# Optimization experiments

Hardware: AMD Instinct MI355X
Metric: run time of the kernel (lower is better)

## Reference

```python
import jax, jax.numpy as jnp
import numpy as np

B, N, COUT, CIN, H, W = 16, 4, 256, 256, 64, 64


def setup_inputs() -> dict:
    key = jax.random.key(0)
    k1, k2, k3, k4 = jax.random.split(key, 4)
    x = jax.random.normal(k1, (B, CIN, H, W), jnp.float32)
    alphas = jax.random.uniform(k2, (B, N), jnp.float32)          # routing weights (lambdas)
    angles = jax.random.normal(k3, (B, N), jnp.float32) * 0.5     # thetas, mixed signs
    # kaiming_normal_(mode='fan_out', relu): std = sqrt(2 / (Cout * k * k))
    std = np.sqrt(2.0 / (COUT * 9)).astype(np.float32)
    weight = jax.random.normal(k4, (N, COUT, CIN, 3, 3), jnp.float32) * std
    return {"x": x, "alphas": alphas, "angles": angles, "weight": weight}


def _rot_mats(thetas):
    """thetas: [M] -> rotation matrices [M, 9, 9] (row, col), matching torch builder."""
    xc = jnp.cos(thetas)
    ys = jnp.sin(thetas)
    a = xc - ys
    b = xc * ys
    c = xc + ys
    z = jnp.zeros_like(xc)
    o = jnp.ones_like(xc)

    def mat(rows):
        # rows: list of 9 lists of 9 [M]-arrays -> [M, 9, 9]
        return jnp.stack([jnp.stack(r, axis=-1) for r in rows], axis=-2)

    pos = mat([
        [a, 1 - a, z, z, z, z, z, z, z],
        [z, xc - b, b, z, 1 - c + b, ys - b, z, z, z],
        [z, z, a, z, z, 1 - a, z, z, z],
        [b, ys - b, z, xc - b, 1 - c + b, z, z, z, z],
        [z, z, z, z, o, z, z, z, z],
        [z, z, z, z, 1 - c + b, xc - b, z, ys - b, b],
        [z, z, z, 1 - a, z, z, a, z, z],
        [z, z, z, ys - b, 1 - c + b, z, b, xc - b, z],
        [z, z, z, z, z, z, z, 1 - a, a],
    ])
    neg = mat([
        [c, z, z, 1 - c, z, z, z, z, z],
        [-b, xc + b, z, b - ys, 1 - a - b, z, z, z, z],
        [z, 1 - c, c, z, z, z, z, z, z],
        [z, z, z, xc + b, 1 - a - b, z, -b, b - ys, z],
        [z, z, z, z, o, z, z, z, z],
        [z, b - ys, -b, z, 1 - a - b, xc + b, z, z, z],
        [z, z, z, z, z, z, c, 1 - c, z],
        [z, z, z, z, 1 - a - b, b - ys, z, xc + b, -b],
        [z, z, z, z, z, 1 - c, z, z, c],
    ])
    m = (thetas >= 0).astype(thetas.dtype)[:, None, None]
    return m * pos + (1 - m) * neg


def reference(x, alphas, angles, weight):
    bsz, Cin, h, w = x.shape
    n, Cout = weight.shape[0], weight.shape[1]
    # [bsz, n, 9, 9] rotation matrices scaled by routing lambdas
    rm = _rot_mats(angles.reshape(-1)).reshape(bsz, n, 9, 9)
    rm = rm * alphas[:, :, None, None]
    # weights [n, Cout, Cin, 3, 3] -> [n, 9, Cout*Cin]
    Wf = weight.transpose(0, 3, 4, 1, 2).reshape(n, 9, Cout * Cin)
    # mix over kernel_number n and source tap q -> per-sample rotated kernels
    rw = jnp.einsum('bnpq,nqm->bpm', rm, Wf)          # [bsz, 9, Cout*Cin]
    rw = rw.reshape(bsz, 3, 3, Cout, Cin).transpose(0, 3, 4, 1, 2)
    rw = rw.reshape(bsz * Cout, Cin, 3, 3)
    # per-sample conv via grouped conv on flattened batch
    xr = x.reshape(1, bsz * Cin, h, w)
    out = jax.lax.conv_general_dilated(
        xr, rw, window_strides=(1, 1), padding=((1, 1), (1, 1)),
        dimension_numbers=('NCHW', 'OIHW', 'NCHW'), feature_group_count=bsz)
    return out.reshape(bsz, Cout, out.shape[2], out.shape[3])
```

## Files before the change

kernel.cpp:

```cpp
#include <hip/hip_runtime.h>
#include <hip/hip_bf16.h>

#define B_    16
#define N_    4
#define COUT  256
#define CIN   256
#define H_    64
#define W_    64
#define K_TOT (CIN * 9)
#define HW    (H_ * W_)
#define NKT   72
#define PAD   66
#define PLANE (PAD * PAD)

typedef __attribute__((ext_vector_type(8))) short short8;
typedef __attribute__((ext_vector_type(4))) float f32x4;
typedef unsigned short ushort_t;

static __device__ __forceinline__ ushort_t f2bf(float f) {
    __hip_bfloat16 h = __float2bfloat16(f);
    return *reinterpret_cast<ushort_t*>(&h);
}

typedef __attribute__((address_space(3))) unsigned int lds_u32;
typedef __attribute__((address_space(1))) const unsigned int glb_u32;
static __device__ __forceinline__ void gl_lds16(const ushort_t* g, ushort_t* l) {
    __builtin_amdgcn_global_load_lds((glb_u32*)g, (lds_u32*)l, 16, 0, 0);
}

#define BARRIER() asm volatile("s_barrier" ::: "memory")
#define VMCNTN(N) asm volatile("s_waitcnt vmcnt(" #N ")" ::: "memory")

__global__ void rot_mats_kernel(const float* __restrict__ alphas,
                                const float* __restrict__ angles,
                                float* __restrict__ rm) {
    int i = threadIdx.x;
    if (i >= B_ * N_) return;
    float th = angles[i], al = alphas[i];
    float xc = cosf(th), ys = sinf(th);
    float a = xc - ys, b = xc * ys, c = xc + ys;
    float r[81];
#pragma unroll
    for (int j = 0; j < 81; ++j) r[j] = 0.f;
    if (th >= 0.f) {
        r[0] = a;          r[1] = 1.f - a;
        r[10] = xc - b;    r[11] = b;        r[13] = 1.f - c + b; r[14] = ys - b;
        r[20] = a;         r[23] = 1.f - a;
        r[27] = b;         r[28] = ys - b;   r[30] = xc - b;      r[31] = 1.f - c + b;
        r[40] = 1.f;
        r[49] = 1.f - c + b; r[50] = xc - b; r[52] = ys - b;      r[53] = b;
        r[57] = 1.f - a;   r[60] = a;
        r[66] = ys - b;    r[67] = 1.f - c + b; r[69] = b;        r[70] = xc - b;
        r[79] = 1.f - a;   r[80] = a;
    } else {
        r[0] = c;          r[3] = 1.f - c;
        r[9] = -b;         r[10] = xc + b;   r[12] = b - ys;      r[13] = 1.f - a - b;
        r[19] = 1.f - c;   r[20] = c;
        r[30] = xc + b;    r[31] = 1.f - a - b; r[33] = -b;       r[34] = b - ys;
        r[40] = 1.f;
        r[46] = b - ys;    r[47] = -b;       r[49] = 1.f - a - b; r[50] = xc + b;
        r[60] = c;         r[61] = 1.f - c;
        r[67] = 1.f - a - b; r[68] = b - ys; r[70] = xc + b;      r[71] = -b;
        r[77] = 1.f - c;   r[80] = c;
    }
#pragma unroll
    for (int j = 0; j < 81; ++j) rm[i * 81 + j] = r[j] * al;
}

__global__ __launch_bounds__(256)
void build_rw_kernel(const float* __restrict__ weight,
                     const float* __restrict__ rm,
                     ushort_t* __restrict__ rw) {
    __shared__ float rms[N_ * 81];
    int tid = threadIdx.x;
    int b = blockIdx.y;
    for (int j = tid; j < N_ * 81; j += 256)
        rms[j] = rm[b * N_ * 81 + j];
    __syncthreads();

    int idx = blockIdx.x * 256 + tid;
    int cout = idx >> 8, cin = idx & 255;

    float wv[N_][9];
#pragma unroll
    for (int n = 0; n < N_; ++n)
#pragma unroll
        for (int q = 0; q < 9; ++q)
            wv[n][q] = weight[(size_t)(n * (COUT * CIN) + idx) * 9 + q];

    ushort_t* dst = rw + (size_t)(b * COUT + cout) * K_TOT + cin;
#pragma unroll
    for (int p = 0; p < 9; ++p) {
        float s = 0.f;
#pragma unroll
        for (int n = 0; n < N_; ++n)
#pragma unroll
            for (int q = 0; q < 9; ++q)
                s += rms[n * 81 + p * 9 + q] * wv[n][q];
        dst[p * 256] = f2bf(s);
    }
}

__global__ __launch_bounds__(256)
void halo_zero_kernel(ushort_t* __restrict__ xt) {
    ushort_t* base = xt + (size_t)blockIdx.x * PLANE * 64;
    int t = threadIdx.x;
    for (int i = t; i < 260; i += 256) {
        int py, px;
        if (i < 66)       { py = 0;  px = i; }
        else if (i < 132) { py = 65; px = i - 66; }
        else if (i < 196) { py = i - 132 + 1; px = 0; }
        else              { py = i - 196 + 1; px = 65; }
        ushort_t* d = base + (size_t)(py * PAD + px) * 64;
        int4 z = {0, 0, 0, 0};
#pragma unroll
        for (int q = 0; q < 8; ++q) *(int4*)(d + q * 8) = z;
    }
}

__global__ __launch_bounds__(256)
void nhwc_kernel(const float* __restrict__ x, ushort_t* __restrict__ xt) {
    int y    = blockIdx.x;
    int cb32 = blockIdx.y;
    int b    = blockIdx.z;
    __shared__ ushort_t tileT[64][40];
    int t = threadIdx.x;

    int ci = t & 31, seg = t >> 5;
    const float* src = x + ((size_t)(b * CIN + cb32 * 32 + ci) * HW + y * 64 + seg * 8);
    float4 f0 = ((const float4*)src)[0];
    float4 f1 = ((const float4*)src)[1];
#pragma unroll
    for (int q = 0; q < 4; ++q) tileT[seg * 8 + q][ci]     = f2bf(((float*)&f0)[q]);
#pragma unroll
    for (int q = 0; q < 4; ++q) tileT[seg * 8 + 4 + q][ci] = f2bf(((float*)&f1)[q]);
    __syncthreads();

    int px = t >> 2, cseg = t & 3;
    ushort_t* dst = xt + ((size_t)(b * 4 + (cb32 >> 1)) * PLANE + (y + 1) * PAD + px + 1) * 64
                       + (cb32 & 1) * 32 + cseg * 8;
    *(int4*)dst = *(const int4*)&tileT[px][cseg * 8];
}

__global__ __launch_bounds__(512, 2)
void conv_kernel(const ushort_t* __restrict__ xt,
                 const ushort_t* __restrict__ rw,
                 float* __restrict__ out) {
    int bid0 = blockIdx.x;
    int bid = (bid0 & 7) * 32 + (bid0 >> 3);
    int b     = bid >> 4;
    int ptile = bid & 15;
    int y0 = ptile * 4;
    int tid = threadIdx.x;
    int lane = tid & 63, wid = tid >> 6;
    int wm = wid >> 2, wn = wid & 3;
    int rA = lane & 15, kseg = lane >> 4;

    __shared__ __align__(16) ushort_t As[3][8192];
    __shared__ __align__(16) ushort_t Bs[3][8192];
    ushort_t* AsB = &As[0][0];
    ushort_t* BsB = &Bs[0][0];

    f32x4 acc[8][4] = {};

    const ushort_t* rwb = rw + (size_t)b * COUT * K_TOT;
    const ushort_t* xtb = xt + ((size_t)b * 4 * PLANE + (size_t)y0 * PAD) * 64;

    int asrc[2], bsrc[2], uDst[2];
#pragma unroll
    for (int i = 0; i < 2; ++i) {
        int u = i * 512 + tid;
        int l = u >> 3, s = u & 7;
        int c = s ^ (l & 7);
        int row = 2 * l + (c >> 2);
        asrc[i] = row * K_TOT + (c & 3) * 8;
        bsrc[i] = ((row >> 6) * PAD + (row & 63)) * 64 + (c & 3) * 8;
        uDst[i] = u * 8;
    }
    const int slotR = (kseg + 4 * (rA & 1)) ^ ((rA >> 1) & 7);
    const int aRd = (wm * 64 + (rA >> 1)) * 64 + slotR * 8;
    const int bRd = (wn * 32 + (rA >> 1)) * 64 + slotR * 8;

#define STAGE_A(KT, Q)                                                         \
    {                                                                          \
        int p_ = (KT) >> 3, sub_ = (KT) & 7;                                   \
        int ako = p_ * 256 + sub_ * 32;                                        \
        gl_lds16(rwb + asrc[0] + ako, AsB + (Q) * 8192 + uDst[0]);             \
        gl_lds16(rwb + asrc[1] + ako, AsB + (Q) * 8192 + uDst[1]);             \
    }

#define STAGE_B(KT, Q)                                                         \
    {                                                                          \
        int p_ = (KT) >> 3, sub_ = (KT) & 7;                                   \
        int ph_ = p_ / 3, pw_ = p_ - 3 * ph_;                                  \
        const ushort_t* sb_ = xtb + (size_t)((sub_ >> 1) * PLANE + ph_ * PAD + pw_) * 64 \
                              + (sub_ & 1) * 32;                               \
        gl_lds16(sb_ + bsrc[0], BsB + (Q) * 8192 + uDst[0]);                   \
        gl_lds16(sb_ + bsrc[1], BsB + (Q) * 8192 + uDst[1]);                   \
    }

#define DO_MFMA(MH)                                                            \
    __builtin_amdgcn_s_setprio(1);                                             \
    _Pragma("unroll")                                                          \
    for (int mi = 0; mi < 4; ++mi)                                             \
        _Pragma("unroll")                                                      \
        for (int ni = 0; ni < 4; ++ni)                                         \
            acc[(MH) * 4 + mi][ni] = __builtin_amdgcn_mfma_f32_16x16x32_bf16(  \
                af[mi], bf[ni], acc[(MH) * 4 + mi][ni], 0, 0, 0);              \
    __builtin_amdgcn_s_setprio(0);

    STAGE_A(0, 0); STAGE_B(0, 0);
    STAGE_A(1, 1); STAGE_B(1, 1);
    VMCNTN(4);
    BARRIER();

    short8 af[4], bf[4];
    int qc = 0;
    for (int kt = 0; kt < NKT; ++kt) {
        int qs = qc + 2; if (qs >= 3) qs -= 3;
        bool more = (kt + 2 < NKT);
#pragma unroll
        for (int mi = 0; mi < 4; ++mi)
            af[mi] = *(const short8*)(AsB + qc * 8192 + aRd + mi * 512);
#pragma unroll
        for (int ni = 0; ni < 4; ++ni)
            bf[ni] = *(const short8*)(BsB + qc * 8192 + bRd + ni * 512);
        if (more) STAGE_A(kt + 2, qs);
        BARRIER();
        DO_MFMA(0);
        BARRIER();
#pragma unroll
        for (int mi = 0; mi < 4; ++mi)
            af[mi] = *(const short8*)(AsB + qc * 8192 + aRd + (mi + 4) * 512);
        if (more) STAGE_B(kt + 2, qs);
        BARRIER();
        DO_MFMA(1);
        if (kt <= NKT - 3)      { VMCNTN(4); }
        else if (kt == NKT - 2) { VMCNTN(0); }
        BARRIER();
        qc = (qc == 2) ? 0 : qc + 1;
    }
#undef STAGE_A
#undef STAGE_B
#undef DO_MFMA

    int row0 = (lane >> 4) * 4;
    int col  = lane & 15;
    float* outb = out + (size_t)b * COUT * HW + ptile * 256;
#pragma unroll
    for (int am = 0; am < 8; ++am)
#pragma unroll
        for (int an = 0; an < 4; ++an)
#pragma unroll
            for (int rr = 0; rr < 4; ++rr) {
                int m = wm * 128 + am * 16 + row0 + rr;
                int n = wn * 64 + an * 16 + col;
                outb[(size_t)m * HW + n] = acc[am][an][rr];
            }
}

extern "C" void kernel_launch(void* const* d_in, const int* in_sizes, int n_in,
                              void* d_out, int out_size, void* d_ws, size_t ws_size,
                              hipStream_t stream) {
    const float* x      = (const float*)d_in[0];
    const float* alphas = (const float*)d_in[1];
    const float* angles = (const float*)d_in[2];
    const float* weight = (const float*)d_in[3];
    float* out = (float*)d_out;

    ushort_t* rw = (ushort_t*)d_ws;
    ushort_t* xt = (ushort_t*)((char*)d_ws + (size_t)B_ * COUT * K_TOT * 2);
    float*    rm = (float*)((char*)d_ws + (size_t)B_ * COUT * K_TOT * 2
                                        + (size_t)64 * PLANE * 64 * 2);

    rot_mats_kernel<<<1, 64, 0, stream>>>(alphas, angles, rm);
    build_rw_kernel<<<dim3(COUT * CIN / 256, B_), 256, 0, stream>>>(weight, rm, rw);
    halo_zero_kernel<<<64, 256, 0, stream>>>(xt);
    nhwc_kernel<<<dim3(64, 8, B_), 256, 0, stream>>>(x, xt);
    conv_kernel<<<256, 512, 0, stream>>>(xt, rw, out);
}
```

Before: 121.5 us.

## Double-buffer MFMA fragments in registers and merge A/B staging per tile

Reworks the conv GEMM main loop so each K-tile reads all eight A and four B fragments from LDS for the next tile into a second register set while the current tile's MFMAs run. A and B global-to-LDS staging now go out together, and the loop needs one wait plus barrier per tile instead of four barriers split across two half-tiles. The loop is unrolled by two to alternate the fragment register sets. The launch bound drops to one block per SM to make room for the extra registers. The cost is less occupancy and a full vmcnt(0) drain every tile, which may expose global load latency.

```diff
diff --git a/kernel.cpp b/kernel.cpp
--- a/kernel.cpp
+++ b/kernel.cpp
@@ -142,7 +142,7 @@
     *(int4*)dst = *(const int4*)&tileT[px][cseg * 8];
 }
 
-__global__ __launch_bounds__(512, 2)
+__global__ __launch_bounds__(512, 1)
 void conv_kernel(const ushort_t* __restrict__ xt,
                  const ushort_t* __restrict__ rw,
                  float* __restrict__ out) {
@@ -181,17 +181,12 @@
     const int aRd = (wm * 64 + (rA >> 1)) * 64 + slotR * 8;
     const int bRd = (wn * 32 + (rA >> 1)) * 64 + slotR * 8;
 
-#define STAGE_A(KT, Q)                                                         \
+#define STAGE_AB(KT, Q)                                                        \
     {                                                                          \
         int p_ = (KT) >> 3, sub_ = (KT) & 7;                                   \
         int ako = p_ * 256 + sub_ * 32;                                        \
         gl_lds16(rwb + asrc[0] + ako, AsB + (Q) * 8192 + uDst[0]);             \
         gl_lds16(rwb + asrc[1] + ako, AsB + (Q) * 8192 + uDst[1]);             \
-    }
-
-#define STAGE_B(KT, Q)                                                         \
-    {                                                                          \
-        int p_ = (KT) >> 3, sub_ = (KT) & 7;                                   \
         int ph_ = p_ / 3, pw_ = p_ - 3 * ph_;                                  \
         const ushort_t* sb_ = xtb + (size_t)((sub_ >> 1) * PLANE + ph_ * PAD + pw_) * 64 \
                               + (sub_ & 1) * 32;                               \
@@ -199,50 +194,51 @@
         gl_lds16(sb_ + bsrc[1], BsB + (Q) * 8192 + uDst[1]);                   \
     }
 
-#define DO_MFMA(MH)                                                            \
-    __builtin_amdgcn_s_setprio(1);                                             \
+#define READ_FRAGS(Q, AF, BF)                                                  \
     _Pragma("unroll")                                                          \
-    for (int mi = 0; mi < 4; ++mi)                                             \
+    for (int mi = 0; mi < 8; ++mi)                                             \
+        AF[mi] = *(const short8*)(AsB + (Q) * 8192 + aRd + mi * 512);          \
+    _Pragma("unroll")                                                          \
+    for (int ni = 0; ni < 4; ++ni)                                             \
+        BF[ni] = *(const short8*)(BsB + (Q) * 8192 + bRd + ni * 512);
+
+#define TILE_BODY(KT, QN, QS, AFC, BFC, AFN, BFN)                              \
+    {                                                                          \
+        if ((KT) + 1 < NKT) { READ_FRAGS(QN, AFN, BFN); }                      \
+        if ((KT) + 2 < NKT) { STAGE_AB((KT) + 2, QS); }                        \
+        __builtin_amdgcn_s_setprio(1);                                         \
         _Pragma("unroll")                                                      \
-        for (int ni = 0; ni < 4; ++ni)                                         \
-            acc[(MH) * 4 + mi][ni] = __builtin_amdgcn_mfma_f32_16x16x32_bf16(  \
-                af[mi], bf[ni], acc[(MH) * 4 + mi][ni], 0, 0, 0);              \
-    __builtin_amdgcn_s_setprio(0);
-
-    STAGE_A(0, 0); STAGE_B(0, 0);
-    STAGE_A(1, 1); STAGE_B(1, 1);
-    VMCNTN(4);
+        for (int mi = 0; mi < 8; ++mi)                                         \
+            _Pragma("unroll")                                                  \
+            for (int ni = 0; ni < 4; ++ni)                                     \
+                acc[mi][ni] = __builtin_amdgcn_mfma_f32_16x16x32_bf16(         \
+                    AFC[mi], BFC[ni], acc[mi][ni], 0, 0, 0);                   \
+        __builtin_amdgcn_s_setprio(0);                                         \
+        VMCNTN(0);                                                             \
+        BARRIER();                                                             \
+    }
+
+    STAGE_AB(0, 0);
+    STAGE_AB(1, 1);
+    VMCNTN(0);
     BARRIER();
 
-    short8 af[4], bf[4];
+    short8 afA[8], bfA[4], afB[8], bfB[4];
+    READ_FRAGS(0, afA, bfA);
+
     int qc = 0;
-    for (int kt = 0; kt < NKT; ++kt) {
+    for (int kt = 0; kt < NKT; kt += 2) {
+        int qn = qc + 1; if (qn >= 3) qn -= 3;
         int qs = qc + 2; if (qs >= 3) qs -= 3;
-        bool more = (kt + 2 < NKT);
-#pragma unroll
-        for (int mi = 0; mi < 4; ++mi)
-            af[mi] = *(const short8*)(AsB + qc * 8192 + aRd + mi * 512);
-#pragma unroll
-        for (int ni = 0; ni < 4; ++ni)
-            bf[ni] = *(const short8*)(BsB + qc * 8192 + bRd + ni * 512);
-        if (more) STAGE_A(kt + 2, qs);
-        BARRIER();
-        DO_MFMA(0);
-        BARRIER();
-#pragma unroll
-        for (int mi = 0; mi < 4; ++mi)
-            af[mi] = *(const short8*)(AsB + qc * 8192 + aRd + (mi + 4) * 512);
-        if (more) STAGE_B(kt + 2, qs);
-        BARRIER();
-        DO_MFMA(1);
-        if (kt <= NKT - 3)      { VMCNTN(4); }
-        else if (kt == NKT - 2) { VMCNTN(0); }
-        BARRIER();
-        qc = (qc == 2) ? 0 : qc + 1;
-    }
-#undef STAGE_A
-#undef STAGE_B
-#undef DO_MFMA
+        TILE_BODY(kt, qn, qs, afA, bfA, afB, bfB);
+        int qn2 = qs;
+        int qs2 = qc;
+        TILE_BODY(kt + 1, qn2, qs2, afB, bfB, afA, bfA);
+        qc = qs;
+    }
+#undef TILE_BODY
+#undef READ_FRAGS
+#undef STAGE_AB
 
     int row0 = (lane >> 4) * 4;
     int col  = lane & 15;
```

New measurement: 117.1 us. 3.6% less time.
